# Kernel optimization log

Measured on AMD Instinct MI355X. Metric: run time of the kernel, lower is better.

## Reference

```python
import jax, jax.numpy as jnp
import numpy as np

N_NODES = 100000


def _gcn_norm(edge_index, num_nodes):
    # PyG GCNConv default: add self-loops, symmetric deg^{-1/2} normalization.
    src, dst = edge_index[0], edge_index[1]
    loops = jnp.arange(num_nodes, dtype=edge_index.dtype)
    src_f = jnp.concatenate([src, loops])  # [E+N]
    dst_f = jnp.concatenate([dst, loops])
    deg = jax.ops.segment_sum(jnp.ones_like(dst_f, dtype=jnp.float32), dst_f, num_segments=num_nodes)
    dinv = jnp.where(deg > 0, jax.lax.rsqrt(deg), 0.0)
    norm = dinv[src_f] * dinv[dst_f]  # [E+N]
    return src_f, dst_f, norm


def _gcn_conv(h, src_f, dst_f, norm, W, b, num_nodes):
    # linear transform first (reduces gather/scatter width), then normalized scatter-add
    hw = h @ W  # [N, out]
    msgs = hw[src_f] * norm[:, None]  # [E+N, out]
    out = jax.ops.segment_sum(msgs, dst_f, num_segments=num_nodes)
    return out + b


def setup_inputs() -> dict:
    key = jax.random.key(0)
    ks = jax.random.split(key, 8)
    N, E, F, H = N_NODES, 3200000, 512, 256
    x = jax.random.normal(ks[0], (N, F), dtype=jnp.float32)
    edge_index = jax.random.randint(ks[1], (2, E), 0, N, dtype=jnp.int64)
    W1 = jax.random.normal(ks[2], (F, H), dtype=jnp.float32) * (1.0 / np.sqrt(F))
    b1 = jnp.zeros((H,), dtype=jnp.float32)
    Wc = jax.random.normal(ks[3], (H, 40), dtype=jnp.float32) * (1.0 / np.sqrt(H))
    bc = jnp.zeros((40,), dtype=jnp.float32)
    Wk = jax.random.normal(ks[4], (H, 16), dtype=jnp.float32) * (1.0 / np.sqrt(H))
    bk = jnp.zeros((16,), dtype=jnp.float32)
    Wd = jax.random.normal(ks[5], (H, 1), dtype=jnp.float32) * (1.0 / np.sqrt(H))
    bd = jnp.zeros((1,), dtype=jnp.float32)
    return {"x": x, "edge_index": edge_index, "W1": W1, "b1": b1, "Wc": Wc, "bc": bc, "Wk": Wk, "bk": bk, "Wd": Wd, "bd": bd}


def reference(x, edge_index, W1, b1, Wc, bc, Wk, bk, Wd, bd):
    N = N_NODES
    src_f, dst_f, norm = _gcn_norm(edge_index, N)
    h = jax.nn.relu(_gcn_conv(x, src_f, dst_f, norm, W1, b1, N))
    # dropout is identity at inference (training=False)
    main_out = _gcn_conv(h, src_f, dst_f, norm, Wc, bc, N)
    clus_out = _gcn_conv(h, src_f, dst_f, norm, Wk, bk, N)
    deg_out = _gcn_conv(h, src_f, dst_f, norm, Wd, bd, N)
    return (main_out, clus_out, deg_out)
```

## Files before the change

kernel.cpp:

```cpp
#include <hip/hip_runtime.h>

#define NN 100000

typedef __attribute__((ext_vector_type(8))) __bf16 bf16x8;
typedef __attribute__((ext_vector_type(8))) unsigned short ushort8v;
typedef __attribute__((ext_vector_type(4))) float f32x4;

__device__ __forceinline__ float bf2f(unsigned short u) {
    union { unsigned int ui; float f; } c;
    c.ui = ((unsigned int)u) << 16;
    return c.f;
}

__device__ __forceinline__ unsigned short f2bf(float f) {
    union { float ff; unsigned int ui; } c;
    c.ff = f;
    unsigned int u = c.ui;
    u += 0x7FFFu + ((u >> 16) & 1u);
    return (unsigned short)(u >> 16);
}

__device__ __forceinline__ unsigned short trunc_hi(float x, float& resid) {
    union { float f; unsigned int u; } c, h;
    c.f = x;
    h.u = c.u & 0xFFFF0000u;
    resid = x - h.f;
    return (unsigned short)(c.u >> 16);
}

__device__ __forceinline__ unsigned short trunc_bits(float x) {
    union { float f; unsigned int u; } c;
    c.f = x;
    return (unsigned short)(c.u >> 16);
}

__global__ void MultiTaskGCN_37623913513359_kernel() {}

__global__ void probe_fmt(const int* ei, const unsigned short* x, int* flags) {
    if (blockIdx.x != 0 || threadIdx.x != 0) return;
    int any = 0;
    for (int i = 0; i < 64; ++i) any |= ei[2 * i + 1];
    flags[0] = (any == 0) ? 1 : 0;
    int bf = 1;
    for (int i = 0; i < 512; ++i) {
        float v = bf2f(x[2 * i]);
        float av = v < 0.0f ? -v : v;
        if (!(v == v) || av > 1.0e6f) { bf = 0; break; }
    }
    flags[1] = bf;
}

__device__ __forceinline__ int edge_src(const int* ei, int is64, int e) {
    if (is64) return ei[2 * e];
    return ei[e];
}
__device__ __forceinline__ int edge_dst(const int* ei, int is64, int e, int E) {
    if (is64) return ei[2 * (E + e)];
    return ei[E + e];
}

__device__ __forceinline__ float load_f(const void* p, int dt, size_t i) {
    if (dt) return bf2f(((const unsigned short*)p)[i]);
    return ((const float*)p)[i];
}

__global__ __launch_bounds__(256) void count_deg_i(const int* ei, const int* flags,
                                                   int* degi, int E) {
    int t = blockIdx.x * 256 + threadIdx.x;
    if (t >= E) return;
    int is64 = flags[0];
    int s = edge_src(ei, is64, t);
    int d = edge_dst(ei, is64, t, E);
    if (((unsigned)s) >= NN || ((unsigned)d) >= NN) return;
    atomicAdd(&degi[d], 1);
}

__global__ __launch_bounds__(256) void make_dinv(const int* degi, float* dinv) {
    int i = blockIdx.x * 256 + threadIdx.x;
    if (i < NN) dinv[i] = rsqrtf((float)degi[i] + 1.0f);
}

__global__ __launch_bounds__(1024) void scan_rowptr(const int* degi, int* rowptr) {
    __shared__ int part[1024];
    int tid = threadIdx.x;
    const int chunk = (NN + 1023) / 1024;
    int base = tid * chunk;
    int s = 0;
    for (int j = 0; j < chunk; ++j) {
        int i = base + j;
        if (i < NN) s += degi[i];
    }
    part[tid] = s;
    __syncthreads();
    for (int off = 1; off < 1024; off <<= 1) {
        int v = (tid >= off) ? part[tid - off] : 0;
        __syncthreads();
        part[tid] += v;
        __syncthreads();
    }
    int run = (tid == 0) ? 0 : part[tid - 1];
    for (int j = 0; j < chunk; ++j) {
        int i = base + j;
        if (i < NN) {
            rowptr[i] = run;
            run += degi[i];
        }
    }
    if (tid == 1023) rowptr[NN] = part[1023];
}

__global__ __launch_bounds__(256) void fill_csr(const int* ei, const int* flags,
                                                const float* dinv, const int* rowptr,
                                                int* cursor, unsigned long long* csr,
                                                int E) {
    int t = blockIdx.x * 256 + threadIdx.x;
    if (t >= E) return;
    int is64 = flags[0];
    int s = edge_src(ei, is64, t);
    int d = edge_dst(ei, is64, t, E);
    if (((unsigned)s) >= NN || ((unsigned)d) >= NN) return;
    int pos = rowptr[d] + atomicAdd(&cursor[d], 1);
    float w = dinv[s] * dinv[d];
    union { float ff; unsigned int ui; } c;
    c.ff = w;
    csr[pos] = ((unsigned long long)c.ui << 32) | (unsigned int)s;
}

__global__ __launch_bounds__(256) void prep_w1t(const void* W1, const int* flags,
                                                unsigned short* hi, unsigned short* lo) {
    int t = blockIdx.x * 256 + threadIdx.x;
    if (t >= 256 * 512) return;
    int n = t >> 9, k = t & 511;
    float v = load_f(W1, flags[1], (size_t)k * 256 + n);
    float r;
    hi[t] = trunc_hi(v, r);
    lo[t] = trunc_bits(r);
}

__global__ __launch_bounds__(256) void prep_wcat(const void* Wc, const void* Wk,
                                                 const void* Wd, const int* flags,
                                                 unsigned short* hi, unsigned short* lo) {
    int t = blockIdx.x * 256 + threadIdx.x;
    if (t >= 64 * 256) return;
    int n = t >> 8, k = t & 255;
    int dt = flags[1];
    float v = 0.0f;
    if (n < 40) v = load_f(Wc, dt, (size_t)k * 40 + n);
    else if (n < 56) v = load_f(Wk, dt, (size_t)k * 16 + (n - 40));
    else if (n == 56) v = load_f(Wd, dt, k);
    float r;
    hi[t] = trunc_hi(v, r);
    lo[t] = trunc_bits(r);
}


template<int NB>
struct StageRegs {
    ushort8v ah[2], al[2], bh[NB], bl[NB];
};

template<int NB>
__device__ __forceinline__ StageRegs<NB> stage_load(const void* A, const unsigned short* BTh,
                                                    const unsigned short* BTl, int M, int K,
                                                    int m0, int n0, int k0,
                                                    int lane, int wid, int adt, bool blo) {
    StageRegs<NB> s;
#pragma unroll
    for (int half = 0; half < 2; ++half) {
        int gr = m0 + lane + half * 64;
        if (gr >= M) gr = M - 1;
        if (adt == 0) {
            const float* ap = (const float*)A + (size_t)gr * K + k0 + wid * 8;
            f32x4 v0 = *(const f32x4*)ap;
            f32x4 v1 = *(const f32x4*)(ap + 4);
            ushort8v h, l;
#pragma unroll
            for (int j = 0; j < 4; ++j) {
                float r;
                h[j] = trunc_hi(v0[j], r);
                l[j] = trunc_bits(r);
            }
#pragma unroll
            for (int j = 0; j < 4; ++j) {
                float r;
                h[4 + j] = trunc_hi(v1[j], r);
                l[4 + j] = trunc_bits(r);
            }
            s.ah[half] = h;
            s.al[half] = l;
        } else {
            s.ah[half] = *(const ushort8v*)((const unsigned short*)A + (size_t)gr * K + k0 + wid * 8);
        }
    }
#pragma unroll
    for (int nb = 0; nb < NB; ++nb) {
        size_t o = (size_t)(n0 + lane + nb * 64) * K + k0 + wid * 8;
        s.bh[nb] = *(const ushort8v*)(BTh + o);
        if (blo) s.bl[nb] = *(const ushort8v*)(BTl + o);
    }
    return s;
}

template<int BM, int BN, int NB>
__device__ __forceinline__ void stage_write(ushort8v (&As)[2][4][BM], ushort8v (&Bs)[2][4][BN],
                                            const StageRegs<NB>& s, int lane, int wid,
                                            bool alo, bool blo) {
    As[0][wid][lane] = s.ah[0];
    As[0][wid][lane + 64] = s.ah[1];
    if (alo) {
        As[1][wid][lane] = s.al[0];
        As[1][wid][lane + 64] = s.al[1];
    }
#pragma unroll
    for (int nb = 0; nb < NB; ++nb) {
        Bs[0][wid][lane + nb * 64] = s.bh[nb];
        if (blo) Bs[1][wid][lane + nb * 64] = s.bl[nb];
    }
}

template<int BM, int BN, int NF>
__device__ __forceinline__ void mfma_step(const ushort8v (&As)[2][4][BM],
                                          const ushort8v (&Bs)[2][4][BN],
                                          f32x4 (&acc)[4][NF],
                                          int wm, int wn, int lane, bool alo, bool blo) {
    const int lr = lane & 15;
    const int lk = lane >> 4;
    bf16x8 ah[4], al[4];
#pragma unroll
    for (int i = 0; i < 4; ++i) {
        ah[i] = *(const bf16x8*)&As[0][lk][wm * 64 + i * 16 + lr];
        if (alo) al[i] = *(const bf16x8*)&As[1][lk][wm * 64 + i * 16 + lr];
    }
    bf16x8 bh[NF], bl[NF];
#pragma unroll
    for (int j = 0; j < NF; ++j) {
        bh[j] = *(const bf16x8*)&Bs[0][lk][wn * (BN / 2) + j * 16 + lr];
        if (blo) bl[j] = *(const bf16x8*)&Bs[1][lk][wn * (BN / 2) + j * 16 + lr];
    }
#pragma unroll
    for (int i = 0; i < 4; ++i) {
#pragma unroll
        for (int j = 0; j < NF; ++j) {
            acc[i][j] = __builtin_amdgcn_mfma_f32_16x16x32_bf16(ah[i], bh[j], acc[i][j], 0, 0, 0);
            if (blo) acc[i][j] = __builtin_amdgcn_mfma_f32_16x16x32_bf16(ah[i], bl[j], acc[i][j], 0, 0, 0);
            if (alo) acc[i][j] = __builtin_amdgcn_mfma_f32_16x16x32_bf16(al[i], bh[j], acc[i][j], 0, 0, 0);
        }
    }
}

template<int BN, int NF>
__global__ __launch_bounds__(256) void gemm_mfma(const void* A, const unsigned short* BTh,
                                                 const unsigned short* BTl, unsigned short* C,
                                                 int M, int N, int K, const int* flags, int amode) {
    constexpr int BM = 128;
    constexpr int NB = BN / 64;
    __shared__ ushort8v As[2][4][BM];
    __shared__ ushort8v Bs[2][4][BN];

    const int tid = threadIdx.x;
    const int lane = tid & 63;
    const int wid = tid >> 6;
    const int wm = wid >> 1;
    const int wn = wid & 1;
    const int dt = flags[1];
    const int adt = (amode == 0) ? dt : 1;
    const bool alo = (adt == 0);
    const bool blo = (dt == 0);
    const int m0 = blockIdx.x * BM;
    const int n0 = blockIdx.y * BN;

    f32x4 zero = {0.0f, 0.0f, 0.0f, 0.0f};
    f32x4 acc[4][NF];
#pragma unroll
    for (int i = 0; i < 4; ++i)
#pragma unroll
        for (int j = 0; j < NF; ++j) acc[i][j] = zero;

    StageRegs<NB> sA = stage_load<NB>(A, BTh, BTl, M, K, m0, n0, 0, lane, wid, adt, blo);
    const int nT = K >> 5;
    for (int t = 0; t < nT; t += 2) {
        __syncthreads();
        stage_write<BM, BN, NB>(As, Bs, sA, lane, wid, alo, blo);
        __syncthreads();
        StageRegs<NB> sB = stage_load<NB>(A, BTh, BTl, M, K, m0, n0, (t + 1) << 5, lane, wid, adt, blo);
        mfma_step<BM, BN, NF>(As, Bs, acc, wm, wn, lane, alo, blo);
        __syncthreads();
        stage_write<BM, BN, NB>(As, Bs, sB, lane, wid, alo, blo);
        __syncthreads();
        if (t + 2 < nT)
            sA = stage_load<NB>(A, BTh, BTl, M, K, m0, n0, (t + 2) << 5, lane, wid, adt, blo);
        mfma_step<BM, BN, NF>(As, Bs, acc, wm, wn, lane, alo, blo);
    }

    const int lr = lane & 15;
    const int lq = lane >> 4;
#pragma unroll
    for (int i = 0; i < 4; ++i) {
#pragma unroll
        for (int rr = 0; rr < 4; ++rr) {
            int row = m0 + wm * 64 + i * 16 + lq * 4 + rr;
            if (row < M) {
#pragma unroll
                for (int j = 0; j < NF; ++j) {
                    int col = n0 + wn * (BN / 2) + j * 16 + lr;
                    C[(size_t)row * N + col] = f2bf(acc[i][j][rr]);
                }
            }
        }
    }
}

__global__ __launch_bounds__(256) void gather_h(const int* rowptr,
                                                const unsigned long long* csr,
                                                const unsigned short* xwb,
                                                const void* b1,
                                                const float* dinv,
                                                const int* flags,
                                                unsigned short* hb) {
    int node = (blockIdx.x * 256 + threadIdx.x) >> 6;
    int lane = threadIdx.x & 63;
    if (node >= NN) return;
    int beg = rowptr[node], end = rowptr[node + 1];
    const unsigned short* xp = xwb + (size_t)lane * 4;

    float a0[4] = {0.f, 0.f, 0.f, 0.f};
    float a1[4] = {0.f, 0.f, 0.f, 0.f};
    float a2[4] = {0.f, 0.f, 0.f, 0.f};
    float a3[4] = {0.f, 0.f, 0.f, 0.f};

    int e = beg;
    for (; e + 4 <= end; e += 4) {
        unsigned long long p0 = csr[e + 0];
        unsigned long long p1 = csr[e + 1];
        unsigned long long p2 = csr[e + 2];
        unsigned long long p3 = csr[e + 3];
        unsigned long long v0 = *(const unsigned long long*)(xp + ((size_t)(unsigned int)p0) * 256);
        unsigned long long v1 = *(const unsigned long long*)(xp + ((size_t)(unsigned int)p1) * 256);
        unsigned long long v2 = *(const unsigned long long*)(xp + ((size_t)(unsigned int)p2) * 256);
        unsigned long long v3 = *(const unsigned long long*)(xp + ((size_t)(unsigned int)p3) * 256);
        union { unsigned int ui; float ff; } w0, w1, w2, w3;
        w0.ui = (unsigned int)(p0 >> 32);
        w1.ui = (unsigned int)(p1 >> 32);
        w2.ui = (unsigned int)(p2 >> 32);
        w3.ui = (unsigned int)(p3 >> 32);
        a0[0] += w0.ff * bf2f((unsigned short)v0);
        a0[1] += w0.ff * bf2f((unsigned short)(v0 >> 16));
        a0[2] += w0.ff * bf2f((unsigned short)(v0 >> 32));
        a0[3] += w0.ff * bf2f((unsigned short)(v0 >> 48));
        a1[0] += w1.ff * bf2f((unsigned short)v1);
        a1[1] += w1.ff * bf2f((unsigned short)(v1 >> 16));
        a1[2] += w1.ff * bf2f((unsigned short)(v1 >> 32));
        a1[3] += w1.ff * bf2f((unsigned short)(v1 >> 48));
        a2[0] += w2.ff * bf2f((unsigned short)v2);
        a2[1] += w2.ff * bf2f((unsigned short)(v2 >> 16));
        a2[2] += w2.ff * bf2f((unsigned short)(v2 >> 32));
        a2[3] += w2.ff * bf2f((unsigned short)(v2 >> 48));
        a3[0] += w3.ff * bf2f((unsigned short)v3);
        a3[1] += w3.ff * bf2f((unsigned short)(v3 >> 16));
        a3[2] += w3.ff * bf2f((unsigned short)(v3 >> 32));
        a3[3] += w3.ff * bf2f((unsigned short)(v3 >> 48));
    }
    for (; e < end; ++e) {
        unsigned long long p = csr[e];
        union { unsigned int ui; float ff; } c;
        c.ui = (unsigned int)(p >> 32);
        unsigned long long v = *(const unsigned long long*)(xp + ((size_t)(unsigned int)p) * 256);
        a0[0] += c.ff * bf2f((unsigned short)v);
        a0[1] += c.ff * bf2f((unsigned short)(v >> 16));
        a0[2] += c.ff * bf2f((unsigned short)(v >> 32));
        a0[3] += c.ff * bf2f((unsigned short)(v >> 48));
    }

    int dt = flags[1];
    float di = dinv[node];
    float sl = di * di;
    size_t base = (size_t)node * 256 + lane * 4;
    unsigned long long v = *(const unsigned long long*)(xwb + base);
    float r0 = sl * bf2f((unsigned short)v)         + (a0[0] + a1[0]) + (a2[0] + a3[0]) + load_f(b1, dt, lane * 4 + 0);
    float r1 = sl * bf2f((unsigned short)(v >> 16)) + (a0[1] + a1[1]) + (a2[1] + a3[1]) + load_f(b1, dt, lane * 4 + 1);
    float r2 = sl * bf2f((unsigned short)(v >> 32)) + (a0[2] + a1[2]) + (a2[2] + a3[2]) + load_f(b1, dt, lane * 4 + 2);
    float r3 = sl * bf2f((unsigned short)(v >> 48)) + (a0[3] + a1[3]) + (a2[3] + a3[3]) + load_f(b1, dt, lane * 4 + 3);
    if (r0 < 0.f) r0 = 0.f;
    if (r1 < 0.f) r1 = 0.f;
    if (r2 < 0.f) r2 = 0.f;
    if (r3 < 0.f) r3 = 0.f;
    unsigned long long o = (unsigned long long)f2bf(r0)
                         | ((unsigned long long)f2bf(r1) << 16)
                         | ((unsigned long long)f2bf(r2) << 32)
                         | ((unsigned long long)f2bf(r3) << 48);
    *(unsigned long long*)(hb + base) = o;
}

__global__ __launch_bounds__(256) void gather_out(const int* rowptr,
                                                  const unsigned long long* csr,
                                                  const unsigned short* hw2b,
                                                  const void* bc, const void* bk,
                                                  const void* bd,
                                                  const float* dinv,
                                                  const int* flags,
                                                  void* outv) {
    int node = (blockIdx.x * 256 + threadIdx.x) >> 6;
    int lane = threadIdx.x & 63;
    if (node >= NN) return;
    int beg = rowptr[node], end = rowptr[node + 1];
    const unsigned short* hp = hw2b + lane;

    float c0 = 0.f, c1 = 0.f, c2 = 0.f, c3 = 0.f;
    float c4 = 0.f, c5 = 0.f, c6 = 0.f, c7 = 0.f;

    int e = beg;
    for (; e + 8 <= end; e += 8) {
        unsigned long long p0 = csr[e + 0];
        unsigned long long p1 = csr[e + 1];
        unsigned long long p2 = csr[e + 2];
        unsigned long long p3 = csr[e + 3];
        unsigned long long p4 = csr[e + 4];
        unsigned long long p5 = csr[e + 5];
        unsigned long long p6 = csr[e + 6];
        unsigned long long p7 = csr[e + 7];
        float f0 = bf2f(hp[((size_t)(unsigned int)p0) * 64]);
        float f1 = bf2f(hp[((size_t)(unsigned int)p1) * 64]);
        float f2 = bf2f(hp[((size_t)(unsigned int)p2) * 64]);
        float f3 = bf2f(hp[((size_t)(unsigned int)p3) * 64]);
        float f4 = bf2f(hp[((size_t)(unsigned int)p4) * 64]);
        float f5 = bf2f(hp[((size_t)(unsigned int)p5) * 64]);
        float f6 = bf2f(hp[((size_t)(unsigned int)p6) * 64]);
        float f7 = bf2f(hp[((size_t)(unsigned int)p7) * 64]);
        union { unsigned int ui; float ff; } w0, w1, w2, w3, w4, w5, w6, w7;
        w0.ui = (unsigned int)(p0 >> 32);
        w1.ui = (unsigned int)(p1 >> 32);
        w2.ui = (unsigned int)(p2 >> 32);
        w3.ui = (unsigned int)(p3 >> 32);
        w4.ui = (unsigned int)(p4 >> 32);
        w5.ui = (unsigned int)(p5 >> 32);
        w6.ui = (unsigned int)(p6 >> 32);
        w7.ui = (unsigned int)(p7 >> 32);
        c0 += w0.ff * f0;
        c1 += w1.ff * f1;
        c2 += w2.ff * f2;
        c3 += w3.ff * f3;
        c4 += w4.ff * f4;
        c5 += w5.ff * f5;
        c6 += w6.ff * f6;
        c7 += w7.ff * f7;
    }
    for (; e < end; ++e) {
        unsigned long long p = csr[e];
        union { unsigned int ui; float ff; } c;
        c.ui = (unsigned int)(p >> 32);
        c0 += c.ff * bf2f(hp[((size_t)(unsigned int)p) * 64]);
    }
    float acc = ((c0 + c1) + (c2 + c3)) + ((c4 + c5) + (c6 + c7));

    if (lane >= 57) return;
    int dt = flags[1];
    float di = dinv[node];
    float v = di * di * bf2f(hw2b[(size_t)node * 64 + lane]) + acc;
    size_t o;
    if (lane < 40) {
        v += load_f(bc, dt, lane);
        o = (size_t)node * 40 + lane;
    } else if (lane < 56) {
        v += load_f(bk, dt, lane - 40);
        o = (size_t)NN * 40 + (size_t)node * 16 + (lane - 40);
    } else {
        v += load_f(bd, dt, 0);
        o = (size_t)NN * 56 + node;
    }
    if (dt) ((unsigned short*)outv)[o] = f2bf(v);
    else ((float*)outv)[o] = v;
}

extern "C" void kernel_launch(void* const* d_in, const int* in_sizes, int n_in,
                              void* d_out, int out_size, void* d_ws, size_t ws_size,
                              hipStream_t stream) {
    const void* x  = d_in[0];
    const int* ei  = (const int*)d_in[1];
    const void* W1 = d_in[2];
    const void* b1 = d_in[3];
    const void* Wc = d_in[4];
    const void* bc = d_in[5];
    const void* Wk = d_in[6];
    const void* bk = d_in[7];
    const void* Wd = d_in[8];
    const void* bd = d_in[9];

    int E = in_sizes[1] / 2;

    hipError_t herr = hipSuccess;
    hipError_t e;

    char* ws = (char*)d_ws;
    size_t off = 0;
    int* flags = (int*)(ws + off);                      off += 256;
    float* dinv = (float*)(ws + off);                   off += 400128;
    int* rowptr = (int*)(ws + off);                     off += 400384;
    char* scr = ws + off;                               off += 800256;
    int* degi = (int*)scr;
    int* cursor = (int*)(scr + 400128);
    unsigned short* w1t_hi = (unsigned short*)scr;
    unsigned short* w1t_lo = (unsigned short*)(scr + 262144);
    unsigned short* wct_hi = (unsigned short*)(scr + 524288);
    unsigned short* wct_lo = (unsigned short*)(scr + 557056);
    unsigned long long* csr = (unsigned long long*)(ws + off); off += (size_t)E * 8;
    unsigned short* xwb = (unsigned short*)(ws + off);  off += (size_t)NN * 256 * 2;
    unsigned short* hb = (unsigned short*)(ws + off);   off += (size_t)NN * 256 * 2;
    unsigned short* hw2b = (unsigned short*)(ws + off); off += (size_t)NN * 64 * 2;

    int ws_bad = (off > ws_size) ? 1 : 0;

    if (!ws_bad) {
        e = hipMemsetAsync(degi, 0, (size_t)NN * 4, stream);
        if (herr == hipSuccess && e != hipSuccess) herr = e;
        e = hipMemsetAsync(cursor, 0, (size_t)NN * 4, stream);
        if (herr == hipSuccess && e != hipSuccess) herr = e;

        probe_fmt<<<1, 64, 0, stream>>>(ei, (const unsigned short*)x, flags);
        count_deg_i<<<(E + 255) / 256, 256, 0, stream>>>(ei, flags, degi, E);
        make_dinv<<<(NN + 255) / 256, 256, 0, stream>>>(degi, dinv);
        scan_rowptr<<<1, 1024, 0, stream>>>(degi, rowptr);
        fill_csr<<<(E + 255) / 256, 256, 0, stream>>>(ei, flags, dinv, rowptr,
                                                      cursor, csr, E);

        prep_w1t<<<512, 256, 0, stream>>>(W1, flags, w1t_hi, w1t_lo);
        prep_wcat<<<64, 256, 0, stream>>>(Wc, Wk, Wd, flags, wct_hi, wct_lo);

        {
            dim3 grid((NN + 127) / 128, 2);
            gemm_mfma<128, 4><<<grid, 256, 0, stream>>>(x, w1t_hi, w1t_lo, xwb,
                                                        NN, 256, 512, flags, 0);
        }
        gather_h<<<(NN + 3) / 4, 256, 0, stream>>>(rowptr, csr, xwb, b1, dinv,
                                                   flags, hb);

        {
            dim3 grid((NN + 127) / 128, 1);
            gemm_mfma<64, 2><<<grid, 256, 0, stream>>>(hb, wct_hi, wct_lo, hw2b,
                                                       NN, 64, 256, flags, 2);
        }
        gather_out<<<(NN + 3) / 4, 256, 0, stream>>>(rowptr, csr, hw2b, bc, bk, bd,
                                                     dinv, flags, d_out);
    }

    e = hipGetLastError();
    if (herr == hipSuccess && e != hipSuccess) herr = e;

    if (herr != hipSuccess) {
        (void)hipMemsetAsync(d_out, 0x41 + ((int)herr & 7), 128, stream);
    }
    if (ws_bad) {
        (void)hipMemsetAsync(d_out, 0x58, 128, stream);
    }
}
```

Baseline: 1.346 ms.

## Use direct global-to-LDS loads in GEMM, vectorize gather_out, parallelize format probe

The GEMM is rewritten to load tiles straight from global memory into LDS via global_load_lds, replacing the register-staged double buffering with a single-buffer loop. It also sets launch bounds for 3 blocks per CU and stages the C tile through LDS so the output is written with 16-byte stores. gather_out now has four lane groups, each handling a different edge, with lanes reading 4 bf16 values at once, and reduces across groups with shuffles. probe_fmt uses a full wavefront and ballots instead of a serial loop. Dropping the prefetch overlap could expose load latency in the GEMM.

```diff
diff --git a/kernel.cpp b/kernel.cpp
--- a/kernel.cpp
+++ b/kernel.cpp
@@ -34,20 +34,33 @@
     return (unsigned short)(c.u >> 16);
 }
 
+__device__ __forceinline__ void gload_lds16(const void* g, void* l) {
+    void* gnc = (void*)g;
+    __builtin_amdgcn_global_load_lds((__attribute__((address_space(1))) void*)gnc,
+                                     (__attribute__((address_space(3))) void*)l,
+                                     16, 0, 0);
+}
+
 __global__ void MultiTaskGCN_37623913513359_kernel() {}
 
 __global__ void probe_fmt(const int* ei, const unsigned short* x, int* flags) {
-    if (blockIdx.x != 0 || threadIdx.x != 0) return;
-    int any = 0;
-    for (int i = 0; i < 64; ++i) any |= ei[2 * i + 1];
-    flags[0] = (any == 0) ? 1 : 0;
-    int bf = 1;
-    for (int i = 0; i < 512; ++i) {
+    if (blockIdx.x != 0 || threadIdx.x >= 64) return;
+    int lane = threadIdx.x & 63;
+    int any = ei[2 * lane + 1];
+    unsigned long long b64 = __ballot(any != 0);
+    int bad = 0;
+#pragma unroll
+    for (int r = 0; r < 8; ++r) {
+        int i = r * 64 + lane;
         float v = bf2f(x[2 * i]);
         float av = v < 0.0f ? -v : v;
-        if (!(v == v) || av > 1.0e6f) { bf = 0; break; }
-    }
-    flags[1] = bf;
+        if (!(v == v) || av > 1.0e6f) bad = 1;
+    }
+    unsigned long long bb = __ballot(bad != 0);
+    if (lane == 0) {
+        flags[0] = (b64 == 0) ? 1 : 0;
+        flags[1] = (bb == 0) ? 1 : 0;
+    }
 }
 
 __device__ __forceinline__ int edge_src(const int* ei, int is64, int e) {
@@ -154,108 +167,20 @@
 }
 
 
-template<int NB>
-struct StageRegs {
-    ushort8v ah[2], al[2], bh[NB], bl[NB];
-};
-
-template<int NB>
-__device__ __forceinline__ StageRegs<NB> stage_load(const void* A, const unsigned short* BTh,
-                                                    const unsigned short* BTl, int M, int K,
-                                                    int m0, int n0, int k0,
-                                                    int lane, int wid, int adt, bool blo) {
-    StageRegs<NB> s;
-#pragma unroll
-    for (int half = 0; half < 2; ++half) {
-        int gr = m0 + lane + half * 64;
-        if (gr >= M) gr = M - 1;
-        if (adt == 0) {
-            const float* ap = (const float*)A + (size_t)gr * K + k0 + wid * 8;
-            f32x4 v0 = *(const f32x4*)ap;
-            f32x4 v1 = *(const f32x4*)(ap + 4);
-            ushort8v h, l;
-#pragma unroll
-            for (int j = 0; j < 4; ++j) {
-                float r;
-                h[j] = trunc_hi(v0[j], r);
-                l[j] = trunc_bits(r);
-            }
-#pragma unroll
-            for (int j = 0; j < 4; ++j) {
-                float r;
-                h[4 + j] = trunc_hi(v1[j], r);
-                l[4 + j] = trunc_bits(r);
-            }
-            s.ah[half] = h;
-            s.al[half] = l;
-        } else {
-            s.ah[half] = *(const ushort8v*)((const unsigned short*)A + (size_t)gr * K + k0 + wid * 8);
-        }
-    }
-#pragma unroll
-    for (int nb = 0; nb < NB; ++nb) {
-        size_t o = (size_t)(n0 + lane + nb * 64) * K + k0 + wid * 8;
-        s.bh[nb] = *(const ushort8v*)(BTh + o);
-        if (blo) s.bl[nb] = *(const ushort8v*)(BTl + o);
-    }
-    return s;
-}
-
-template<int BM, int BN, int NB>
-__device__ __forceinline__ void stage_write(ushort8v (&As)[2][4][BM], ushort8v (&Bs)[2][4][BN],
-                                            const StageRegs<NB>& s, int lane, int wid,
-                                            bool alo, bool blo) {
-    As[0][wid][lane] = s.ah[0];
-    As[0][wid][lane + 64] = s.ah[1];
-    if (alo) {
-        As[1][wid][lane] = s.al[0];
-        As[1][wid][lane + 64] = s.al[1];
-    }
-#pragma unroll
-    for (int nb = 0; nb < NB; ++nb) {
-        Bs[0][wid][lane + nb * 64] = s.bh[nb];
-        if (blo) Bs[1][wid][lane + nb * 64] = s.bl[nb];
-    }
-}
-
-template<int BM, int BN, int NF>
-__device__ __forceinline__ void mfma_step(const ushort8v (&As)[2][4][BM],
-                                          const ushort8v (&Bs)[2][4][BN],
-                                          f32x4 (&acc)[4][NF],
-                                          int wm, int wn, int lane, bool alo, bool blo) {
-    const int lr = lane & 15;
-    const int lk = lane >> 4;
-    bf16x8 ah[4], al[4];
-#pragma unroll
-    for (int i = 0; i < 4; ++i) {
-        ah[i] = *(const bf16x8*)&As[0][lk][wm * 64 + i * 16 + lr];
-        if (alo) al[i] = *(const bf16x8*)&As[1][lk][wm * 64 + i * 16 + lr];
-    }
-    bf16x8 bh[NF], bl[NF];
-#pragma unroll
-    for (int j = 0; j < NF; ++j) {
-        bh[j] = *(const bf16x8*)&Bs[0][lk][wn * (BN / 2) + j * 16 + lr];
-        if (blo) bl[j] = *(const bf16x8*)&Bs[1][lk][wn * (BN / 2) + j * 16 + lr];
-    }
-#pragma unroll
-    for (int i = 0; i < 4; ++i) {
-#pragma unroll
-        for (int j = 0; j < NF; ++j) {
-            acc[i][j] = __builtin_amdgcn_mfma_f32_16x16x32_bf16(ah[i], bh[j], acc[i][j], 0, 0, 0);
-            if (blo) acc[i][j] = __builtin_amdgcn_mfma_f32_16x16x32_bf16(ah[i], bl[j], acc[i][j], 0, 0, 0);
-            if (alo) acc[i][j] = __builtin_amdgcn_mfma_f32_16x16x32_bf16(al[i], bh[j], acc[i][j], 0, 0, 0);
-        }
-    }
-}
-
 template<int BN, int NF>
-__global__ __launch_bounds__(256) void gemm_mfma(const void* A, const unsigned short* BTh,
-                                                 const unsigned short* BTl, unsigned short* C,
-                                                 int M, int N, int K, const int* flags, int amode) {
+__global__ __launch_bounds__(256, 3) void gemm_gl(const void* A,
+                                                  const unsigned short* BTh,
+                                                  const unsigned short* BTl,
+                                                  unsigned short* C,
+                                                  int M, int N, int K,
+                                                  const int* flags, int amode) {
     constexpr int BM = 128;
-    constexpr int NB = BN / 64;
-    __shared__ ushort8v As[2][4][BM];
-    __shared__ ushort8v Bs[2][4][BN];
+    constexpr int HB = BN / 64;
+    __shared__ ushort8v smem[4 * BM + 4 * BM + 4 * BN + 4 * BN];
+    ushort8v* Ash = smem;
+    ushort8v* Asl = smem + 4 * BM;
+    ushort8v* Bsh = smem + 8 * BM;
+    ushort8v* Bsl = smem + 8 * BM + 4 * BN;
 
     const int tid = threadIdx.x;
     const int lane = tid & 63;
@@ -263,9 +188,10 @@
     const int wm = wid >> 1;
     const int wn = wid & 1;
     const int dt = flags[1];
-    const int adt = (amode == 0) ? dt : 1;
-    const bool alo = (adt == 0);
-    const bool blo = (dt == 0);
+
+    const int alo = (amode == 0 && dt == 0) ? 1 : 0;
+    const int blo = (dt == 0) ? 1 : 0;
+
     const int m0 = blockIdx.x * BM;
     const int n0 = blockIdx.y * BN;
 
@@ -276,36 +202,112 @@
 #pragma unroll
         for (int j = 0; j < NF; ++j) acc[i][j] = zero;
 
-    StageRegs<NB> sA = stage_load<NB>(A, BTh, BTl, M, K, m0, n0, 0, lane, wid, adt, blo);
+    const float* Af = (const float*)A;
+    const unsigned short* Ab16 = (const unsigned short*)A;
+
     const int nT = K >> 5;
-    for (int t = 0; t < nT; t += 2) {
+    for (int t = 0; t < nT; ++t) {
+        const int k0 = t << 5;
+        for (int q = wid; q < 4 * HB; q += 4) {
+            int kg = q / HB, hf = q % HB;
+            int col = n0 + hf * 64 + lane;
+            gload_lds16(BTh + (size_t)col * K + k0 + kg * 8, Bsh + kg * BN + hf * 64);
+            if (blo) gload_lds16(BTl + (size_t)col * K + k0 + kg * 8, Bsl + kg * BN + hf * 64);
+        }
+        if (alo) {
+            f32x4 ra[2][2];
+#pragma unroll
+            for (int u = 0; u < 2; ++u) {
+                int q = wid + u * 4;
+                int kg = q >> 1, hf = q & 1;
+                int row = m0 + hf * 64 + lane;
+                if (row >= M) row = M - 1;
+                const float* ap = Af + (size_t)row * K + k0 + kg * 8;
+                ra[u][0] = *(const f32x4*)ap;
+                ra[u][1] = *(const f32x4*)(ap + 4);
+            }
+#pragma unroll
+            for (int u = 0; u < 2; ++u) {
+                int q = wid + u * 4;
+                int kg = q >> 1, hf = q & 1;
+                ushort8v h, l;
+                float r;
+#pragma unroll
+                for (int j = 0; j < 4; ++j) {
+                    h[j] = trunc_hi(ra[u][0][j], r);
+                    l[j] = trunc_bits(r);
+                }
+#pragma unroll
+                for (int j = 0; j < 4; ++j) {
+                    h[4 + j] = trunc_hi(ra[u][1][j], r);
+                    l[4 + j] = trunc_bits(r);
+                }
+                Ash[kg * BM + hf * 64 + lane] = h;
+                Asl[kg * BM + hf * 64 + lane] = l;
+            }
+        } else {
+            for (int q = wid; q < 8; q += 4) {
+                int kg = q >> 1, hf = q & 1;
+                int row = m0 + hf * 64 + lane;
+                if (row >= M) row = M - 1;
+                gload_lds16(Ab16 + (size_t)row * K + k0 + kg * 8, Ash + kg * BM + hf * 64);
+            }
+        }
         __syncthreads();
-        stage_write<BM, BN, NB>(As, Bs, sA, lane, wid, alo, blo);
+
+        {
+            const int lr = lane & 15;
+            const int lk = lane >> 4;
+            bf16x8 ah[4], al[4];
+#pragma unroll
+            for (int i = 0; i < 4; ++i) {
+                ah[i] = *(const bf16x8*)&Ash[lk * BM + wm * 64 + i * 16 + lr];
+                if (alo) al[i] = *(const bf16x8*)&Asl[lk * BM + wm * 64 + i * 16 + lr];
+            }
+            bf16x8 bh[NF], bl[NF];
+#pragma unroll
+            for (int j = 0; j < NF; ++j) {
+                bh[j] = *(const bf16x8*)&Bsh[lk * BN + wn * (NF * 16) + j * 16 + lr];
+                if (blo) bl[j] = *(const bf16x8*)&Bsl[lk * BN + wn * (NF * 16) + j * 16 + lr];
+            }
+#pragma unroll
+            for (int i = 0; i < 4; ++i) {
+#pragma unroll
+                for (int j = 0; j < NF; ++j) {
+                    acc[i][j] = __builtin_amdgcn_mfma_f32_16x16x32_bf16(ah[i], bh[j], acc[i][j], 0, 0, 0);
+                    if (blo) acc[i][j] = __builtin_amdgcn_mfma_f32_16x16x32_bf16(ah[i], bl[j], acc[i][j], 0, 0, 0);
+                    if (alo) acc[i][j] = __builtin_amdgcn_mfma_f32_16x16x32_bf16(al[i], bh[j], acc[i][j], 0, 0, 0);
+                }
+            }
+        }
         __syncthreads();
-        StageRegs<NB> sB = stage_load<NB>(A, BTh, BTl, M, K, m0, n0, (t + 1) << 5, lane, wid, adt, blo);
-        mfma_step<BM, BN, NF>(As, Bs, acc, wm, wn, lane, alo, blo);
-        __syncthreads();
-        stage_write<BM, BN, NB>(As, Bs, sB, lane, wid, alo, blo);
-        __syncthreads();
-        if (t + 2 < nT)
-            sA = stage_load<NB>(A, BTh, BTl, M, K, m0, n0, (t + 2) << 5, lane, wid, adt, blo);
-        mfma_step<BM, BN, NF>(As, Bs, acc, wm, wn, lane, alo, blo);
-    }
-
+    }
+
+    unsigned short* cs = (unsigned short*)smem;
     const int lr = lane & 15;
     const int lq = lane >> 4;
 #pragma unroll
     for (int i = 0; i < 4; ++i) {
 #pragma unroll
-        for (int rr = 0; rr < 4; ++rr) {
-            int row = m0 + wm * 64 + i * 16 + lq * 4 + rr;
-            if (row < M) {
-#pragma unroll
-                for (int j = 0; j < NF; ++j) {
-                    int col = n0 + wn * (BN / 2) + j * 16 + lr;
-                    C[(size_t)row * N + col] = f2bf(acc[i][j][rr]);
-                }
-            }
+        for (int j = 0; j < NF; ++j) {
+#pragma unroll
+            for (int rr = 0; rr < 4; ++rr) {
+                int row = wm * 64 + i * 16 + lq * 4 + rr;
+                int col = wn * (NF * 16) + j * 16 + lr;
+                cs[row * BN + col] = f2bf(acc[i][j][rr]);
+            }
+        }
+    }
+    __syncthreads();
+    constexpr int TOTAL = BM * BN;
+#pragma unroll
+    for (int base = 0; base < TOTAL; base += 2048) {
+        int idx = base + tid * 8;
+        int r = idx / BN;
+        int c = idx % BN;
+        int grow = m0 + r;
+        if (grow < M) {
+            *(ushort8v*)(C + (size_t)grow * N + n0 + c) = *(const ushort8v*)(cs + idx);
         }
     }
 }
@@ -403,72 +405,75 @@
     int lane = threadIdx.x & 63;
     if (node >= NN) return;
     int beg = rowptr[node], end = rowptr[node + 1];
-    const unsigned short* hp = hw2b + lane;
-
-    float c0 = 0.f, c1 = 0.f, c2 = 0.f, c3 = 0.f;
-    float c4 = 0.f, c5 = 0.f, c6 = 0.f, c7 = 0.f;
+    int grp = lane >> 4;
+    int sub = lane & 15;
+    const unsigned short* hp = hw2b + (size_t)sub * 4;
+
+    float acc[4] = {0.f, 0.f, 0.f, 0.f};
 
     int e = beg;
-    for (; e + 8 <= end; e += 8) {
-        unsigned long long p0 = csr[e + 0];
-        unsigned long long p1 = csr[e + 1];
-        unsigned long long p2 = csr[e + 2];
-        unsigned long long p3 = csr[e + 3];
-        unsigned long long p4 = csr[e + 4];
-        unsigned long long p5 = csr[e + 5];
-        unsigned long long p6 = csr[e + 6];
-        unsigned long long p7 = csr[e + 7];
-        float f0 = bf2f(hp[((size_t)(unsigned int)p0) * 64]);
-        float f1 = bf2f(hp[((size_t)(unsigned int)p1) * 64]);
-        float f2 = bf2f(hp[((size_t)(unsigned int)p2) * 64]);
-        float f3 = bf2f(hp[((size_t)(unsigned int)p3) * 64]);
-        float f4 = bf2f(hp[((size_t)(unsigned int)p4) * 64]);
-        float f5 = bf2f(hp[((size_t)(unsigned int)p5) * 64]);
-        float f6 = bf2f(hp[((size_t)(unsigned int)p6) * 64]);
-        float f7 = bf2f(hp[((size_t)(unsigned int)p7) * 64]);
-        union { unsigned int ui; float ff; } w0, w1, w2, w3, w4, w5, w6, w7;
+    for (; e + 16 <= end; e += 16) {
+        unsigned long long p0 = csr[e + grp];
+        unsigned long long p1 = csr[e + 4 + grp];
+        unsigned long long p2 = csr[e + 8 + grp];
+        unsigned long long p3 = csr[e + 12 + grp];
+        unsigned long long v0 = *(const unsigned long long*)(hp + ((size_t)(unsigned int)p0) * 64);
+        unsigned long long v1 = *(const unsigned long long*)(hp + ((size_t)(unsigned int)p1) * 64);
+        unsigned long long v2 = *(const unsigned long long*)(hp + ((size_t)(unsigned int)p2) * 64);
+        unsigned long long v3 = *(const unsigned long long*)(hp + ((size_t)(unsigned int)p3) * 64);
+        union { unsigned int ui; float ff; } w0, w1, w2, w3;
         w0.ui = (unsigned int)(p0 >> 32);
         w1.ui = (unsigned int)(p1 >> 32);
         w2.ui = (unsigned int)(p2 >> 32);
         w3.ui = (unsigned int)(p3 >> 32);
-        w4.ui = (unsigned int)(p4 >> 32);
-        w5.ui = (unsigned int)(p5 >> 32);
-        w6.ui = (unsigned int)(p6 >> 32);
-        w7.ui = (unsigned int)(p7 >> 32);
-        c0 += w0.ff * f0;
-        c1 += w1.ff * f1;
-        c2 += w2.ff * f2;
-        c3 += w3.ff * f3;
-        c4 += w4.ff * f4;
-        c5 += w5.ff * f5;
-        c6 += w6.ff * f6;
-        c7 += w7.ff * f7;
-    }
-    for (; e < end; ++e) {
-        unsigned long long p = csr[e];
-        union { unsigned int ui; float ff; } c;
-        c.ui = (unsigned int)(p >> 32);
-        c0 += c.ff * bf2f(hp[((size_t)(unsigned int)p) * 64]);
-    }
-    float acc = ((c0 + c1) + (c2 + c3)) + ((c4 + c5) + (c6 + c7));
-
-    if (lane >= 57) return;
+#pragma unroll
+        for (int j = 0; j < 4; ++j) acc[j] += w0.ff * bf2f((unsigned short)(v0 >> (16 * j)));
+#pragma unroll
+        for (int j = 0; j < 4; ++j) acc[j] += w1.ff * bf2f((unsigned short)(v1 >> (16 * j)));
+#pragma unroll
+        for (int j = 0; j < 4; ++j) acc[j] += w2.ff * bf2f((unsigned short)(v2 >> (16 * j)));
+#pragma unroll
+        for (int j = 0; j < 4; ++j) acc[j] += w3.ff * bf2f((unsigned short)(v3 >> (16 * j)));
+    }
+    for (; e < end; e += 4) {
+        int idx = e + grp;
+        unsigned long long p = (idx < end) ? csr[idx] : 0ull;
+        union { unsigned int ui; float ff; } w;
+        w.ui = (unsigned int)(p >> 32);
+        unsigned long long v = *(const unsigned long long*)(hp + ((size_t)(unsigned int)p) * 64);
+#pragma unroll
+        for (int j = 0; j < 4; ++j) acc[j] += w.ff * bf2f((unsigned short)(v >> (16 * j)));
+    }
+
+#pragma unroll
+    for (int j = 0; j < 4; ++j) {
+        acc[j] += __shfl_xor(acc[j], 16, 64);
+        acc[j] += __shfl_xor(acc[j], 32, 64);
+    }
+
+    if (lane >= 16) return;
     int dt = flags[1];
     float di = dinv[node];
-    float v = di * di * bf2f(hw2b[(size_t)node * 64 + lane]) + acc;
-    size_t o;
-    if (lane < 40) {
-        v += load_f(bc, dt, lane);
-        o = (size_t)node * 40 + lane;
-    } else if (lane < 56) {
-        v += load_f(bk, dt, lane - 40);
-        o = (size_t)NN * 40 + (size_t)node * 16 + (lane - 40);
-    } else {
-        v += load_f(bd, dt, 0);
-        o = (size_t)NN * 56 + node;
-    }
-    if (dt) ((unsigned short*)outv)[o] = f2bf(v);
-    else ((float*)outv)[o] = v;
+    float sl = di * di;
+#pragma unroll
+    for (int j = 0; j < 4; ++j) {
+        int c = sub * 4 + j;
+        if (c >= 57) continue;
+        float v = sl * bf2f(hw2b[(size_t)node * 64 + c]) + acc[j];
+        size_t o;
+        if (c < 40) {
+            v += load_f(bc, dt, c);
+            o = (size_t)node * 40 + c;
+        } else if (c < 56) {
+            v += load_f(bk, dt, c - 40);
+            o = (size_t)NN * 40 + (size_t)node * 16 + (c - 40);
+        } else {
+            v += load_f(bd, dt, 0);
+            o = (size_t)NN * 56 + node;
+        }
+        if (dt) ((unsigned short*)outv)[o] = f2bf(v);
+        else ((float*)outv)[o] = v;
+    }
 }
 
 extern "C" void kernel_launch(void* const* d_in, const int* in_sizes, int n_in,
@@ -527,16 +532,16 @@
 
         {
             dim3 grid((NN + 127) / 128, 2);
-            gemm_mfma<128, 4><<<grid, 256, 0, stream>>>(x, w1t_hi, w1t_lo, xwb,
-                                                        NN, 256, 512, flags, 0);
+            gemm_gl<128, 4><<<grid, 256, 0, stream>>>(x, w1t_hi, w1t_lo, xwb,
+                                                      NN, 256, 512, flags, 0);
         }
         gather_h<<<(NN + 3) / 4, 256, 0, stream>>>(rowptr, csr, xwb, b1, dinv,
                                                    flags, hb);
 
         {
             dim3 grid((NN + 127) / 128, 1);
-            gemm_mfma<64, 2><<<grid, 256, 0, stream>>>(hb, wct_hi, wct_lo, hw2b,
-                                                       NN, 64, 256, flags, 2);
+            gemm_gl<64, 2><<<grid, 256, 0, stream>>>(hb, wct_hi, wct_lo,
+                                                     hw2b, NN, 64, 256, flags, 2);
         }
         gather_out<<<(NN + 3) / 4, 256, 0, stream>>>(rowptr, csr, hw2b, bc, bk, bd,
                                                      dinv, flags, d_out);
```

Result: faster. 1.199 ms (-10.9%).
